# Kernel optimization log

Measured on AMD Instinct MI355X. Metric: run time of the kernel, lower is better.

The kernel has to match this reference:

```python
import jax, jax.numpy as jnp
import numpy as np

LN_EPS = 1e-5

def _mlp(x, W1, b1, W2, b2):
    h = jax.nn.relu(x @ W1 + b1)
    return h @ W2 + b2

def _layernorm(x, g, b):
    mu = jnp.mean(x, axis=-1, keepdims=True)
    var = jnp.var(x, axis=-1, keepdims=True)
    return (x - mu) * jax.lax.rsqrt(var + LN_EPS) * g + b

def setup_inputs() -> dict:
    key = jax.random.key(0)
    ks = jax.random.split(key, 24)
    N, E, G = 50000, 1600000, 64
    F = 32          # all feature widths (edge/node/global, in and out)
    L = 128         # latent_size
    din_e = 2 * F + F + F   # receiver, sender, edge, global = 128
    din_n = F + F + F + F   # node, global, recv-agg, send-agg = 128
    din_g = F + F + F       # node-agg, edge-agg, global = 96
    def w(k, shape, fan_in):
        return jax.random.normal(k, shape, dtype=jnp.float32) / np.sqrt(fan_in)
    inp = {
        "edge_attr": jax.random.normal(ks[0], (E, F), dtype=jnp.float32),
        "node_attr": jax.random.normal(ks[1], (N, F), dtype=jnp.float32),
        "global_attr": jax.random.normal(ks[2], (G, F), dtype=jnp.float32),
        "edge_index": jax.random.randint(ks[3], (2, E), 0, N, dtype=jnp.int32),
        "batch": jnp.sort(jax.random.randint(ks[4], (N,), 0, G, dtype=jnp.int32)),
        # edge MLP + LayerNorm
        "eW1": w(ks[5], (din_e, L), din_e), "eb1": jnp.zeros((L,), jnp.float32),
        "eW2": w(ks[6], (L, F), L),        "eb2": jnp.zeros((F,), jnp.float32),
        "eg": jnp.ones((F,), jnp.float32),  "eB": jnp.zeros((F,), jnp.float32),
        # node MLP + LayerNorm
        "nW1": w(ks[7], (din_n, L), din_n), "nb1": jnp.zeros((L,), jnp.float32),
        "nW2": w(ks[8], (L, F), L),        "nb2": jnp.zeros((F,), jnp.float32),
        "ng": jnp.ones((F,), jnp.float32),  "nB": jnp.zeros((F,), jnp.float32),
        # global MLP (activate_final only, no LayerNorm in GlobalModel)
        "gW1": w(ks[9], (din_g, L), din_g), "gb1": jnp.zeros((L,), jnp.float32),
        "gW2": w(ks[10], (L, F), L),       "gb2": jnp.zeros((F,), jnp.float32),
    }
    return inp

def reference(edge_attr, node_attr, global_attr, edge_index, batch,
              eW1, eb1, eW2, eb2, eg, eB,
              nW1, nb1, nW2, nb2, ng, nB,
              gW1, gb1, gW2, gb2):
    N = node_attr.shape[0]
    G = global_attr.shape[0]
    row, col = edge_index[0], edge_index[1]
    edge_batch = batch[row]                       # [E] graph id per edge

    # --- edge model: gather node/global feats to edges, MLP, ReLU, LN ---
    sender = node_attr[row]                       # [E, F]
    receiver = node_attr[col]                     # [E, F]
    g2e = global_attr[edge_batch]                 # [E, F]
    e_in = jnp.concatenate([receiver, sender, edge_attr, g2e], axis=-1)
    edge_new = _layernorm(jax.nn.relu(_mlp(e_in, eW1, eb1, eW2, eb2)), eg, eB)

    # --- node model: segment-sum edges to nodes, MLP, ReLU, LN ---
    g2n = global_attr[batch]                      # [N, F]
    send_agg = jax.ops.segment_sum(edge_new, row, num_segments=N)
    recv_agg = jax.ops.segment_sum(edge_new, col, num_segments=N)
    n_in = jnp.concatenate([node_attr, g2n, recv_agg, send_agg], axis=-1)
    node_new = _layernorm(jax.nn.relu(_mlp(n_in, nW1, nb1, nW2, nb2)), ng, nB)

    # --- global model: segment-sum nodes & edges to globals, MLP, ReLU ---
    n2g = jax.ops.segment_sum(node_new, batch, num_segments=G)
    e2g = jax.ops.segment_sum(edge_new, edge_batch, num_segments=G)
    g_in = jnp.concatenate([n2g, e2g, global_attr], axis=-1)
    global_new = jax.nn.relu(_mlp(g_in, gW1, gb1, gW2, gb2))

    return edge_new, node_new, global_new
```

## Files before the change

kernel.cpp:

```cpp
#include <hip/hip_runtime.h>
#include <hip/hip_fp16.h>
#include <cstdint>
#include <cstddef>

#define LN_EPS 1e-5f
#define STR 136

typedef unsigned short u16;
typedef unsigned int   u32;
typedef __attribute__((ext_vector_type(8))) short bf16x8;
typedef __attribute__((ext_vector_type(4))) float f32x4;

#define MFMA16 __builtin_amdgcn_mfma_f32_16x16x32_bf16

__device__ __forceinline__ u16 f2bf(float f) {
    u32 x = __float_as_uint(f);
    return (u16)((x + 0x7fffu + ((x >> 16) & 1u)) >> 16);
}
__device__ __forceinline__ u32 pack2(float x, float y) {
    return (u32)f2bf(x) | ((u32)f2bf(y) << 16);
}
__device__ __forceinline__ bf16x8 cvt8(float4 a, float4 b) {
    union { bf16x8 v; u32 w[4]; } u;
    u.w[0] = pack2(a.x, a.y); u.w[1] = pack2(a.z, a.w);
    u.w[2] = pack2(b.x, b.y); u.w[3] = pack2(b.z, b.w);
    return u.v;
}
__device__ __forceinline__ u32 h2_to_bf2(u32 h) {
    __half2 hv = *reinterpret_cast<__half2*>(&h);
    float lo = __half2float(__low2half(hv));
    float hi = __half2float(__high2half(hv));
    return pack2(lo, hi);
}
__device__ __forceinline__ bf16x8 cvtf16x8(uint4 a) {
    union { bf16x8 v; u32 w[4]; } u;
    u.w[0] = h2_to_bf2(a.x); u.w[1] = h2_to_bf2(a.y);
    u.w[2] = h2_to_bf2(a.z); u.w[3] = h2_to_bf2(a.w);
    return u.v;
}

__global__ void prep_kernel(const float* __restrict__ eW1, const float* __restrict__ eW2,
                            const float* __restrict__ nW1, const float* __restrict__ nW2,
                            u16* eW1T, u16* eW2T, u16* nW1T, u16* nW2T)
{
    int idx = blockIdx.x * 256 + threadIdx.x;
    if (idx < 16384) {
        int k = idx >> 7, n = idx & 127;
        eW1T[n * STR + k] = f2bf(eW1[idx]);
        nW1T[n * STR + k] = f2bf(nW1[idx]);
    }
    if (idx < 4096) {
        int k = idx >> 5, n = idx & 31;
        eW2T[n * STR + k] = f2bf(eW2[idx]);
        nW2T[n * STR + k] = f2bf(nW2[idx]);
    }
}

__global__ void cvt_nodes(const float* __restrict__ node_attr,
                          const float* __restrict__ global_attr,
                          u16* __restrict__ nodeB, u16* __restrict__ globB,
                          int n8, int g8)
{
    int stride = gridDim.x * 256;
    for (int i = blockIdx.x * 256 + threadIdx.x; i < n8 + g8; i += stride) {
        const float4* s; uint4* d; int j;
        if (i < n8) { s = (const float4*)node_attr;   d = (uint4*)nodeB; j = i; }
        else        { s = (const float4*)global_attr; d = (uint4*)globB; j = i - n8; }
        float4 a = s[2 * j], b = s[2 * j + 1];
        uint4 o;
        o.x = pack2(a.x, a.y); o.y = pack2(a.z, a.w);
        o.z = pack2(b.x, b.y); o.w = pack2(b.z, b.w);
        d[j] = o;
    }
}

__global__ __launch_bounds__(256, 2)
void edge_mfma(const float* __restrict__ edge_attr,
               const int* __restrict__ edge_index,
               const int* __restrict__ batch,
               const u16* __restrict__ nodeB,
               const u16* __restrict__ globB,
               const u16* __restrict__ W1T, const float* __restrict__ b1,
               const u16* __restrict__ W2T, const float* __restrict__ b2,
               const float* __restrict__ gamma, const float* __restrict__ beta,
               float* __restrict__ edge_out,
               __half* __restrict__ send_agg, __half* __restrict__ recv_agg,
               int E)
{
    __shared__ __align__(16) u16 sW1[128 * STR];
    __shared__ __align__(16) u16 sW2[32 * STR];
    __shared__ __align__(16) u16 sH[4][32 * STR];
    __shared__ int2 sIdx[4][2][32];

    const int tid  = threadIdx.x;
    const int wave = tid >> 6;
    const int lane = tid & 63;
    const int quad = lane >> 4;
    const int ln   = lane & 15;

    {
        const uint4* s1 = reinterpret_cast<const uint4*>(W1T);
        uint4* d1 = reinterpret_cast<uint4*>(sW1);
        for (int i = tid; i < 128 * STR / 8; i += 256) d1[i] = s1[i];
        const uint4* s2 = reinterpret_cast<const uint4*>(W2T);
        uint4* d2 = reinterpret_cast<uint4*>(sW2);
        for (int i = tid; i < 32 * STR / 8; i += 256) d2[i] = s2[i];
    }
    __syncthreads();

    const int totW = gridDim.x * 4;
    const int numTiles = (E + 31) >> 5;
    int tile = blockIdx.x * 4 + wave;
    if (tile >= numTiles) return;

    float bias1[8];
#pragma unroll
    for (int nt = 0; nt < 8; nt++) bias1[nt] = b1[nt * 16 + ln];
    const float g0 = gamma[ln], g1 = gamma[16 + ln];
    const float B0 = beta[ln],  B1 = beta[16 + ln];
    const float bb0 = b2[ln],   bb1 = b2[16 + ln];
    const bool evn = (ln & 1) == 0;
    const int fpair = evn ? ln : (15 + ln);

    u16* H = sH[wave];
    int p = 0;

    auto load_tile = [&](int t, bf16x8 (&af)[2][4], float4 (&pf)[2][2], int2* idxb) {
        long t32 = (long)t * 32;
#pragma unroll
        for (int m = 0; m < 2; m++) {
            long e  = t32 + m * 16 + ln;
            long ec = e < E ? e : (long)E - 1;
            int row = edge_index[ec];
            int col = edge_index[(long)E + ec];
            int gb  = batch[row];
            if (quad == 0) idxb[m * 16 + ln] = make_int2(row, col);
            af[m][0] = *reinterpret_cast<const bf16x8*>(nodeB + (long)col * 32 + quad * 8);
            af[m][1] = *reinterpret_cast<const bf16x8*>(nodeB + (long)row * 32 + quad * 8);
            af[m][3] = *reinterpret_cast<const bf16x8*>(globB + (long)gb * 32 + quad * 8);
            const float4* ea = reinterpret_cast<const float4*>(edge_attr + ec * 32 + quad * 8);
            pf[m][0] = ea[0];
            pf[m][1] = ea[1];
        }
    };

    auto step = [&](bf16x8 (&afC)[2][4], bf16x8 (&afN)[2][4],
                    float4 (&pfC)[2][2], float4 (&pfN)[2][2]) -> bool {
        afC[0][2] = cvt8(pfC[0][0], pfC[0][1]);
        afC[1][2] = cvt8(pfC[1][0], pfC[1][1]);

        const int tnext = tile + totW;
        const bool hn = tnext < numTiles;
        if (hn) load_tile(tnext, afN, pfN, sIdx[wave][p ^ 1]);
        __builtin_amdgcn_sched_barrier(0);

        f32x4 acc1[2][8];
#pragma unroll
        for (int mt = 0; mt < 2; mt++)
#pragma unroll
            for (int nt = 0; nt < 8; nt++) acc1[mt][nt] = (f32x4)0.f;

#pragma unroll
        for (int ks = 0; ks < 4; ks++) {
            const int ko = ks * 32 + quad * 8;
#pragma unroll
            for (int nt = 0; nt < 8; nt++) {
                bf16x8 bw = *reinterpret_cast<const bf16x8*>(sW1 + (nt * 16 + ln) * STR + ko);
                acc1[0][nt] = MFMA16(afC[0][ks], bw, acc1[0][nt], 0, 0, 0);
                acc1[1][nt] = MFMA16(afC[1][ks], bw, acc1[1][nt], 0, 0, 0);
            }
        }

#pragma unroll
        for (int nt = 0; nt < 8; nt++) {
#pragma unroll
            for (int mt = 0; mt < 2; mt++)
#pragma unroll
                for (int r = 0; r < 4; r++) {
                    float h = fmaxf(acc1[mt][nt][r] + bias1[nt], 0.f);
                    H[(mt * 16 + quad * 4 + r) * STR + nt * 16 + ln] = f2bf(h);
                }
        }

        f32x4 acc2[2][2];
#pragma unroll
        for (int mt = 0; mt < 2; mt++)
#pragma unroll
            for (int nt = 0; nt < 2; nt++) acc2[mt][nt] = (f32x4)0.f;

#pragma unroll
        for (int ks = 0; ks < 4; ks++) {
            const int ko = ks * 32 + quad * 8;
            bf16x8 a0 = *reinterpret_cast<const bf16x8*>(H + ln * STR + ko);
            bf16x8 a1 = *reinterpret_cast<const bf16x8*>(H + (16 + ln) * STR + ko);
#pragma unroll
            for (int nt = 0; nt < 2; nt++) {
                bf16x8 bw = *reinterpret_cast<const bf16x8*>(sW2 + (nt * 16 + ln) * STR + ko);
                acc2[0][nt] = MFMA16(a0, bw, acc2[0][nt], 0, 0, 0);
                acc2[1][nt] = MFMA16(a1, bw, acc2[1][nt], 0, 0, 0);
            }
        }

        int2* idxb = sIdx[wave][p];
        const long e0 = (long)tile * 32;
#pragma unroll
        for (int mt = 0; mt < 2; mt++) {
#pragma unroll
            for (int r = 0; r < 4; r++) {
                float v0 = fmaxf(acc2[mt][0][r] + bb0, 0.f);
                float v1 = fmaxf(acc2[mt][1][r] + bb1, 0.f);
                float s = v0 + v1, sq = v0 * v0 + v1 * v1;
#pragma unroll
                for (int m = 1; m < 16; m <<= 1) {
                    s  += __shfl_xor(s,  m, 64);
                    sq += __shfl_xor(sq, m, 64);
                }
                float mean = s * (1.f / 32.f);
                float var  = fmaxf(sq * (1.f / 32.f) - mean * mean, 0.f);
                float rs   = rsqrtf(var + LN_EPS);
                float y0 = (v0 - mean) * rs * g0 + B0;
                float y1 = (v1 - mean) * rs * g1 + B1;
                float p0 = __shfl_xor(y0, 1, 64);
                float p1 = __shfl_xor(y1, 1, 64);
                int rowl = mt * 16 + quad * 4 + r;
                long e = e0 + rowl;
                if (e < E) {
                    __builtin_nontemporal_store(y0, &edge_out[e * 32 + ln]);
                    __builtin_nontemporal_store(y1, &edge_out[e * 32 + 16 + ln]);
                    __half2 val = evn
                        ? __halves2half2(__float2half_rn(y0), __float2half_rn(p0))
                        : __halves2half2(__float2half_rn(p1), __float2half_rn(y1));
                    int2 rc = idxb[rowl];
                    unsafeAtomicAdd(reinterpret_cast<__half2*>(send_agg + (long)rc.x * 32 + fpair), val);
                    unsafeAtomicAdd(reinterpret_cast<__half2*>(recv_agg + (long)rc.y * 32 + fpair), val);
                }
            }
        }
        tile = tnext;
        p ^= 1;
        return hn;
    };

    bf16x8 af0[2][4], af1[2][4];
    float4 pf0[2][2], pf1[2][2];
    load_tile(tile, af0, pf0, sIdx[wave][0]);
    for (;;) {
        if (!step(af0, af1, pf0, pf1)) break;
        if (!step(af1, af0, pf1, pf0)) break;
    }
}

__global__ __launch_bounds__(64, 2)
void node_mfma(const u16* __restrict__ nodeB, const u16* __restrict__ globB,
               const int* __restrict__ batch,
               const __half* __restrict__ send_agg,
               const __half* __restrict__ recv_agg,
               const u16* __restrict__ W1T, const float* __restrict__ b1,
               const u16* __restrict__ W2T, const float* __restrict__ b2,
               const float* __restrict__ gamma, const float* __restrict__ beta,
               float* __restrict__ node_out,
               float* __restrict__ n2g, float* __restrict__ e2g,
               int N)
{
    __shared__ __align__(16) u16 sH[32 * STR];
    __shared__ float sRed[8][64];
    __shared__ int sSlotGb[8];
    __shared__ int sGb[32];

    const int lane = threadIdx.x;
    const int quad = lane >> 4;
    const int ln   = lane & 15;

    for (int i = lane; i < 512; i += 64) ((float*)sRed)[i] = 0.f;
    if (lane < 8) sSlotGb[lane] = -1;

    const long n0 = (long)blockIdx.x * 32;
    const int gbF = batch[n0 < N ? n0 : N - 1];

    bf16x8 af[2][4];
#pragma unroll
    for (int m = 0; m < 2; m++) {
        long n  = n0 + m * 16 + ln;
        long nc = n < N ? n : (long)N - 1;
        int gb  = batch[nc];
        if (quad == 0) sGb[m * 16 + ln] = gb;
        af[m][0] = *reinterpret_cast<const bf16x8*>(nodeB + nc * 32 + quad * 8);
        af[m][1] = *reinterpret_cast<const bf16x8*>(globB + (long)gb * 32 + quad * 8);
        uint4 rv = *reinterpret_cast<const uint4*>(recv_agg + nc * 32 + quad * 8);
        uint4 sv = *reinterpret_cast<const uint4*>(send_agg + nc * 32 + quad * 8);
        af[m][2] = cvtf16x8(rv);
        af[m][3] = cvtf16x8(sv);
    }

    f32x4 acc1[2][8];
#pragma unroll
    for (int mt = 0; mt < 2; mt++)
#pragma unroll
        for (int nt = 0; nt < 8; nt++) acc1[mt][nt] = (f32x4)0.f;

#pragma unroll
    for (int ks = 0; ks < 4; ks++) {
        const int ko = ks * 32 + quad * 8;
#pragma unroll
        for (int nt = 0; nt < 8; nt++) {
            bf16x8 bw = *reinterpret_cast<const bf16x8*>(W1T + (nt * 16 + ln) * STR + ko);
            acc1[0][nt] = MFMA16(af[0][ks], bw, acc1[0][nt], 0, 0, 0);
            acc1[1][nt] = MFMA16(af[1][ks], bw, acc1[1][nt], 0, 0, 0);
        }
    }

#pragma unroll
    for (int nt = 0; nt < 8; nt++) {
        float bias = b1[nt * 16 + ln];
#pragma unroll
        for (int mt = 0; mt < 2; mt++)
#pragma unroll
            for (int r = 0; r < 4; r++) {
                float h = fmaxf(acc1[mt][nt][r] + bias, 0.f);
                sH[(mt * 16 + quad * 4 + r) * STR + nt * 16 + ln] = f2bf(h);
            }
    }

    f32x4 acc2[2][2];
#pragma unroll
    for (int mt = 0; mt < 2; mt++)
#pragma unroll
        for (int nt = 0; nt < 2; nt++) acc2[mt][nt] = (f32x4)0.f;

#pragma unroll
    for (int ks = 0; ks < 4; ks++) {
        const int ko = ks * 32 + quad * 8;
        bf16x8 a0 = *reinterpret_cast<const bf16x8*>(sH + ln * STR + ko);
        bf16x8 a1 = *reinterpret_cast<const bf16x8*>(sH + (16 + ln) * STR + ko);
#pragma unroll
        for (int nt = 0; nt < 2; nt++) {
            bf16x8 bw = *reinterpret_cast<const bf16x8*>(W2T + (nt * 16 + ln) * STR + ko);
            acc2[0][nt] = MFMA16(a0, bw, acc2[0][nt], 0, 0, 0);
            acc2[1][nt] = MFMA16(a1, bw, acc2[1][nt], 0, 0, 0);
        }
    }

    const float g0 = gamma[ln], g1 = gamma[16 + ln];
    const float B0 = beta[ln],  B1 = beta[16 + ln];
    const float bb0 = b2[ln],   bb1 = b2[16 + ln];

#pragma unroll
    for (int mt = 0; mt < 2; mt++) {
#pragma unroll
        for (int r = 0; r < 4; r++) {
            float v0 = fmaxf(acc2[mt][0][r] + bb0, 0.f);
            float v1 = fmaxf(acc2[mt][1][r] + bb1, 0.f);
            float s = v0 + v1, sq = v0 * v0 + v1 * v1;
#pragma unroll
            for (int m = 1; m < 16; m <<= 1) {
                s  += __shfl_xor(s,  m, 64);
                sq += __shfl_xor(sq, m, 64);
            }
            float mean = s * (1.f / 32.f);
            float var  = fmaxf(sq * (1.f / 32.f) - mean * mean, 0.f);
            float rs   = rsqrtf(var + LN_EPS);
            float y0 = (v0 - mean) * rs * g0 + B0;
            float y1 = (v1 - mean) * rs * g1 + B1;
            int rowl = mt * 16 + quad * 4 + r;
            long n = n0 + rowl;
            if (n < N) {
                node_out[n * 32 + ln]      = y0;
                node_out[n * 32 + 16 + ln] = y1;
                int gb = sGb[rowl];
                float sa0 = __half2float(send_agg[n * 32 + ln]);
                float sa1 = __half2float(send_agg[n * 32 + 16 + ln]);
                int slot = gb - gbF;
                if (slot >= 0 && slot < 8) {
                    if (ln == 0) sSlotGb[slot] = gb;
                    atomicAdd(&sRed[slot][ln],      y0);
                    atomicAdd(&sRed[slot][16 + ln], y1);
                    atomicAdd(&sRed[slot][32 + ln], sa0);
                    atomicAdd(&sRed[slot][48 + ln], sa1);
                } else {
                    unsafeAtomicAdd(n2g + (long)gb * 32 + ln,      y0);
                    unsafeAtomicAdd(n2g + (long)gb * 32 + 16 + ln, y1);
                    unsafeAtomicAdd(e2g + (long)gb * 32 + ln,      sa0);
                    unsafeAtomicAdd(e2g + (long)gb * 32 + 16 + ln, sa1);
                }
            }
        }
    }

#pragma unroll 1
    for (int s2 = 0; s2 < 8; s2++) {
        int gb2 = sSlotGb[s2];
        if (gb2 >= 0) {
            float v = sRed[s2][lane];
            float* dst = (lane < 32) ? (n2g + (long)gb2 * 32 + lane)
                                     : (e2g + (long)gb2 * 32 + (lane - 32));
            unsafeAtomicAdd(dst, v);
        }
    }
}

__global__ void global_kernel(const float* __restrict__ n2g,
                              const float* __restrict__ e2g,
                              const float* __restrict__ global_attr,
                              const float* __restrict__ W1, const float* __restrict__ b1,
                              const float* __restrict__ W2, const float* __restrict__ b2,
                              float* __restrict__ out)
{
    __shared__ float gin[96];
    __shared__ float h[128];
    int g = blockIdx.x, t = threadIdx.x;
    if (t < 32) {
        gin[t]      = n2g[g * 32 + t];
        gin[32 + t] = e2g[g * 32 + t];
        gin[64 + t] = global_attr[g * 32 + t];
    }
    __syncthreads();
    float acc = b1[t];
#pragma unroll 1
    for (int k = 0; k < 96; k++) acc = fmaf(gin[k], W1[k * 128 + t], acc);
    h[t] = fmaxf(acc, 0.f);
    __syncthreads();
    if (t < 32) {
        float o = b2[t];
#pragma unroll 1
        for (int j = 0; j < 128; j++) o = fmaf(h[j], W2[j * 32 + t], o);
        out[g * 32 + t] = fmaxf(o, 0.f);
    }
}

extern "C" void kernel_launch(void* const* d_in, const int* in_sizes, int n_in,
                              void* d_out, int out_size, void* d_ws, size_t ws_size,
                              hipStream_t stream)
{
    const float* edge_attr   = (const float*)d_in[0];
    const float* node_attr   = (const float*)d_in[1];
    const float* global_attr = (const float*)d_in[2];
    const int*   edge_index  = (const int*)d_in[3];
    const int*   batch       = (const int*)d_in[4];
    const float* eW1 = (const float*)d_in[5];
    const float* eb1 = (const float*)d_in[6];
    const float* eW2 = (const float*)d_in[7];
    const float* eb2 = (const float*)d_in[8];
    const float* eg  = (const float*)d_in[9];
    const float* eB  = (const float*)d_in[10];
    const float* nW1 = (const float*)d_in[11];
    const float* nb1 = (const float*)d_in[12];
    const float* nW2 = (const float*)d_in[13];
    const float* nb2 = (const float*)d_in[14];
    const float* ng  = (const float*)d_in[15];
    const float* nB  = (const float*)d_in[16];
    const float* gW1 = (const float*)d_in[17];
    const float* gb1 = (const float*)d_in[18];
    const float* gW2 = (const float*)d_in[19];
    const float* gb2 = (const float*)d_in[20];

    const int E = in_sizes[0] / 32;
    const int N = in_sizes[1] / 32;
    const int G = in_sizes[2] / 32;

    float* out      = (float*)d_out;
    float* edge_out = out;
    float* node_out = out + (size_t)E * 32;
    float* glob_out = out + (size_t)(E + N) * 32;

    __half* send_agg = (__half*)d_ws;
    __half* recv_agg = send_agg + (size_t)N * 32;
    float*  n2g      = (float*)(recv_agg + (size_t)N * 32);
    float*  e2g      = n2g + (size_t)G * 32;
    u16* nodeB = (u16*)(e2g + (size_t)G * 32);
    u16* globB = nodeB + (size_t)N * 32;
    u16* eW1T  = globB + (size_t)G * 32;
    u16* eW2T  = eW1T + 128 * STR;
    u16* nW1T  = eW2T + 32 * STR;
    u16* nW2T  = nW1T + 128 * STR;

    size_t zero_bytes = (size_t)N * 32 * 2 * sizeof(__half)
                      + (size_t)G * 32 * 2 * sizeof(float);
    hipMemsetAsync(d_ws, 0, zero_bytes, stream);

    prep_kernel<<<64, 256, 0, stream>>>(eW1, eW2, nW1, nW2, eW1T, eW2T, nW1T, nW2T);
    cvt_nodes<<<784, 256, 0, stream>>>(node_attr, global_attr, nodeB, globB, N * 4, G * 4);

    edge_mfma<<<512, 256, 0, stream>>>(
        edge_attr, edge_index, batch, nodeB, globB,
        eW1T, eb1, eW2T, eb2, eg, eB,
        edge_out, send_agg, recv_agg, E);

    node_mfma<<<(N + 31) / 32, 64, 0, stream>>>(
        nodeB, globB, batch, send_agg, recv_agg,
        nW1T, nb1, nW2T, nb2, ng, nB,
        node_out, n2g, e2g, N);

    global_kernel<<<G, 128, 0, stream>>>(
        n2g, e2g, global_attr, gW1, gb1, gW2, gb2, glob_out);
}
```

Measured before the change: 654.0 us.

## Precompute per-edge graph ids, prefetch edge indices two tiles ahead, keep W2 in registers

A new pre-pass kernel computes each edge's graph id (batch of its sender) into a workspace array. The edge kernel then no longer does a dependent batch[row] lookup before gathering global features. Edge indices are prefetched two tiles ahead while the feature gathers run one tile ahead, which breaks up the chain of dependent loads. The second-layer weights are held in per-lane registers instead of shared memory. The cost is an extra kernel launch, an extra E-sized int buffer written and read, and higher register pressure. edge_attr now sits in a single buffer, so its load for the next tile is less overlapped.

```diff
diff --git a/kernel.cpp b/kernel.cpp
--- a/kernel.cpp
+++ b/kernel.cpp
@@ -74,10 +74,19 @@
     }
 }
 
+__global__ void gbe_kernel(const int* __restrict__ edge_index,
+                           const int* __restrict__ batch,
+                           int* __restrict__ gbE, int E)
+{
+    int stride = gridDim.x * 256;
+    for (int e = blockIdx.x * 256 + threadIdx.x; e < E; e += stride)
+        gbE[e] = batch[edge_index[e]];
+}
+
 __global__ __launch_bounds__(256, 2)
 void edge_mfma(const float* __restrict__ edge_attr,
                const int* __restrict__ edge_index,
-               const int* __restrict__ batch,
+               const int* __restrict__ gbE,
                const u16* __restrict__ nodeB,
                const u16* __restrict__ globB,
                const u16* __restrict__ W1T, const float* __restrict__ b1,
@@ -88,7 +97,6 @@
                int E)
 {
     __shared__ __align__(16) u16 sW1[128 * STR];
-    __shared__ __align__(16) u16 sW2[32 * STR];
     __shared__ __align__(16) u16 sH[4][32 * STR];
     __shared__ int2 sIdx[4][2][32];
 
@@ -102,9 +110,6 @@
         const uint4* s1 = reinterpret_cast<const uint4*>(W1T);
         uint4* d1 = reinterpret_cast<uint4*>(sW1);
         for (int i = tid; i < 128 * STR / 8; i += 256) d1[i] = s1[i];
-        const uint4* s2 = reinterpret_cast<const uint4*>(W2T);
-        uint4* d2 = reinterpret_cast<uint4*>(sW2);
-        for (int i = tid; i < 32 * STR / 8; i += 256) d2[i] = s2[i];
     }
     __syncthreads();
 
@@ -122,22 +127,39 @@
     const bool evn = (ln & 1) == 0;
     const int fpair = evn ? ln : (15 + ln);
 
+    bf16x8 w2f[2][4];
+#pragma unroll
+    for (int nt = 0; nt < 2; nt++)
+#pragma unroll
+        for (int ks = 0; ks < 4; ks++)
+            w2f[nt][ks] = *reinterpret_cast<const bf16x8*>(
+                W2T + (nt * 16 + ln) * STR + ks * 32 + quad * 8);
+
     u16* H = sH[wave];
     int p = 0;
-
-    auto load_tile = [&](int t, bf16x8 (&af)[2][4], float4 (&pf)[2][2], int2* idxb) {
+    float4 pf[2][2];
+
+    auto load_idx = [&](int t, int (&row)[2], int (&col)[2], int (&gb)[2]) {
+#pragma unroll
+        for (int m = 0; m < 2; m++) {
+            long e  = (long)t * 32 + m * 16 + ln;
+            long ec = e < E ? e : (long)E - 1;
+            row[m] = edge_index[ec];
+            col[m] = edge_index[(long)E + ec];
+            gb[m]  = gbE[ec];
+        }
+    };
+    auto load_af = [&](int t, const int (&row)[2], const int (&col)[2], const int (&gb)[2],
+                       bf16x8 (&af)[2][4], int2* idxb) {
         long t32 = (long)t * 32;
 #pragma unroll
         for (int m = 0; m < 2; m++) {
+            if (quad == 0) idxb[m * 16 + ln] = make_int2(row[m], col[m]);
+            af[m][0] = *reinterpret_cast<const bf16x8*>(nodeB + (long)col[m] * 32 + quad * 8);
+            af[m][1] = *reinterpret_cast<const bf16x8*>(nodeB + (long)row[m] * 32 + quad * 8);
+            af[m][3] = *reinterpret_cast<const bf16x8*>(globB + (long)gb[m] * 32 + quad * 8);
             long e  = t32 + m * 16 + ln;
             long ec = e < E ? e : (long)E - 1;
-            int row = edge_index[ec];
-            int col = edge_index[(long)E + ec];
-            int gb  = batch[row];
-            if (quad == 0) idxb[m * 16 + ln] = make_int2(row, col);
-            af[m][0] = *reinterpret_cast<const bf16x8*>(nodeB + (long)col * 32 + quad * 8);
-            af[m][1] = *reinterpret_cast<const bf16x8*>(nodeB + (long)row * 32 + quad * 8);
-            af[m][3] = *reinterpret_cast<const bf16x8*>(globB + (long)gb * 32 + quad * 8);
             const float4* ea = reinterpret_cast<const float4*>(edge_attr + ec * 32 + quad * 8);
             pf[m][0] = ea[0];
             pf[m][1] = ea[1];
@@ -145,13 +167,16 @@
     };
 
     auto step = [&](bf16x8 (&afC)[2][4], bf16x8 (&afN)[2][4],
-                    float4 (&pfC)[2][2], float4 (&pfN)[2][2]) -> bool {
-        afC[0][2] = cvt8(pfC[0][0], pfC[0][1]);
-        afC[1][2] = cvt8(pfC[1][0], pfC[1][1]);
-
-        const int tnext = tile + totW;
-        const bool hn = tnext < numTiles;
-        if (hn) load_tile(tnext, afN, pfN, sIdx[wave][p ^ 1]);
+                    int (&rowF)[2], int (&colF)[2], int (&gbF)[2],
+                    int (&rowN)[2], int (&colN)[2], int (&gbN)[2]) -> bool {
+        afC[0][2] = cvt8(pf[0][0], pf[0][1]);
+        afC[1][2] = cvt8(pf[1][0], pf[1][1]);
+
+        const int t2 = tile + 2 * totW;
+        if (t2 < numTiles) load_idx(t2, rowF, colF, gbF);
+        const int tn = tile + totW;
+        const bool hn = tn < numTiles;
+        if (hn) load_af(tn, rowN, colN, gbN, afN, sIdx[wave][p ^ 1]);
         __builtin_amdgcn_sched_barrier(0);
 
         f32x4 acc1[2][8];
@@ -195,9 +220,8 @@
             bf16x8 a1 = *reinterpret_cast<const bf16x8*>(H + (16 + ln) * STR + ko);
 #pragma unroll
             for (int nt = 0; nt < 2; nt++) {
-                bf16x8 bw = *reinterpret_cast<const bf16x8*>(sW2 + (nt * 16 + ln) * STR + ko);
-                acc2[0][nt] = MFMA16(a0, bw, acc2[0][nt], 0, 0, 0);
-                acc2[1][nt] = MFMA16(a1, bw, acc2[1][nt], 0, 0, 0);
+                acc2[0][nt] = MFMA16(a0, w2f[nt][ks], acc2[0][nt], 0, 0, 0);
+                acc2[1][nt] = MFMA16(a1, w2f[nt][ks], acc2[1][nt], 0, 0, 0);
             }
         }
 
@@ -236,17 +260,20 @@
                 }
             }
         }
-        tile = tnext;
+        tile = tn;
         p ^= 1;
         return hn;
     };
 
-    bf16x8 af0[2][4], af1[2][4];
-    float4 pf0[2][2], pf1[2][2];
-    load_tile(tile, af0, pf0, sIdx[wave][0]);
+    int rowA[2], colA[2], gbA[2], rowB[2], colB[2], gbB[2];
+    bf16x8 afA[2][4], afB[2][4];
+    load_idx(tile, rowA, colA, gbA);
+    if (tile + totW < numTiles) load_idx(tile + totW, rowB, colB, gbB);
+    load_af(tile, rowA, colA, gbA, afA, sIdx[wave][0]);
+
     for (;;) {
-        if (!step(af0, af1, pf0, pf1)) break;
-        if (!step(af1, af0, pf1, pf0)) break;
+        if (!step(afA, afB, rowA, colA, gbA, rowB, colB, gbB)) break;
+        if (!step(afB, afA, rowB, colB, gbB, rowA, colA, gbA)) break;
     }
 }
 
@@ -468,7 +495,8 @@
     float*  e2g      = n2g + (size_t)G * 32;
     u16* nodeB = (u16*)(e2g + (size_t)G * 32);
     u16* globB = nodeB + (size_t)N * 32;
-    u16* eW1T  = globB + (size_t)G * 32;
+    int* gbE   = (int*)(globB + (size_t)G * 32);
+    u16* eW1T  = (u16*)(gbE + (size_t)E);
     u16* eW2T  = eW1T + 128 * STR;
     u16* nW1T  = eW2T + 32 * STR;
     u16* nW2T  = nW1T + 128 * STR;
@@ -479,9 +507,10 @@
 
     prep_kernel<<<64, 256, 0, stream>>>(eW1, eW2, nW1, nW2, eW1T, eW2T, nW1T, nW2T);
     cvt_nodes<<<784, 256, 0, stream>>>(node_attr, global_attr, nodeB, globB, N * 4, G * 4);
+    gbe_kernel<<<2048, 256, 0, stream>>>(edge_index, batch, gbE, E);
 
     edge_mfma<<<512, 256, 0, stream>>>(
-        edge_attr, edge_index, batch, nodeB, globB,
+        edge_attr, edge_index, gbE, nodeB, globB,
         eW1T, eb1, eW2T, eb2, eg, eB,
         edge_out, send_agg, recv_agg, E);
 
```

Result: faster. 634.4 us (-3.0%).
